# Optimization experiments

Hardware: AMD Instinct MI355X
Metric: run time of the kernel (lower is better)

The kernel has to match this reference:

```python
import jax, jax.numpy as jnp
import numpy as np

# smoothing constants (from init_kwargs)
KERNEL_SIZE = 20
WINDOW = (-10.0, 10.0)
SIGMA = 4.0
AMPLITUDE = 0.5
N_SMOOTH = 331  # 350 - 20 + 1


def setup_inputs() -> dict:
    key = jax.random.key(0)
    ks = jax.random.split(key, 6)
    W, A, M, D = 4000, 64, 6, 500
    wavelengths = jnp.linspace(0.3, 2.5, W, dtype=jnp.float32)  # um
    grid = jnp.linspace(0.25, 2.6, D, dtype=jnp.float32)        # material wavelength tables
    n_tab = 1.3 + 1.5 * jax.random.uniform(ks[0], (M, D), dtype=jnp.float32)
    k_tab = 0.05 * jax.random.uniform(ks[1], (M, D), dtype=jnp.float32)
    fixed_data = jnp.stack([jnp.broadcast_to(grid, (M, D)), n_tab, k_tab], axis=1)  # [M,3,D]
    refractive_index = 1.5 + 1.5 * jax.random.uniform(ks[2], (350,), dtype=jnp.float32)
    compression_ratio = jnp.ones((1,), jnp.float32)
    thickness_above_unk = 0.05 + 0.2 * jax.random.uniform(ks[3], (10,), dtype=jnp.float32)  # um
    thickness_below_unk = 0.05 + 0.2 * jax.random.uniform(ks[4], (9,), dtype=jnp.float32)   # um
    angle_of_incidences = jnp.linspace(0.0, 60.0, A, dtype=jnp.float32)  # degrees
    # stack order: incoming | 10 above | unknown (index M) | 9 below | outgoing
    md = [0] + [1, 2] * 5 + [M] + [3, 4] * 4 + [3] + [5]
    material_distribution = jnp.array(md, dtype=jnp.int32)  # [22]
    unknown_layer_thickness = jnp.array([500.0], jnp.float32)  # nm
    return dict(refractive_index=refractive_index, compression_ratio=compression_ratio,
                fixed_data=fixed_data, thickness_above_unk=thickness_above_unk,
                thickness_below_unk=thickness_below_unk, wavelengths=wavelengths,
                angle_of_incidences=angle_of_incidences,
                material_distribution=material_distribution, polarization=0,
                unknown_layer_thickness=unknown_layer_thickness)


def reference(refractive_index, compression_ratio, fixed_data, thickness_above_unk,
              thickness_below_unk, wavelengths, angle_of_incidences,
              material_distribution, polarization, unknown_layer_thickness):
    D = fixed_data.shape[2]
    n_repeat = D - N_SMOOTH
    # --- gaussian smoothing of the unknown layer's refractive index (valid conv) ---
    x = jnp.linspace(WINDOW[0], WINDOW[1], KERNEL_SIZE)
    g = AMPLITUDE * jnp.exp(-0.5 * (x / SIGMA) ** 2)
    g = (g / jnp.sum(g)).astype(refractive_index.dtype)
    nk_s = jnp.convolve(refractive_index, g, mode='valid')            # [331]
    nk = jnp.concatenate([nk_s, jnp.full((n_repeat,), nk_s[-1], nk_s.dtype)])  # pad to max_data_dim
    dyn_wl = jnp.linspace(jnp.min(wavelengths), jnp.max(wavelengths), N_SMOOTH)
    dyn_wl = jnp.concatenate([dyn_wl, jnp.full((n_repeat,), dyn_wl[-1], dyn_wl.dtype)])
    # --- interpolate all material n,k tables onto the experimental wavelengths ---
    interp = jax.vmap(lambda xp, fp: jnp.interp(wavelengths, xp, fp))
    n_fixc = interp(fixed_data[:, 0], fixed_data[:, 1]) + 1j * interp(fixed_data[:, 0], fixed_data[:, 2])  # [M,W]
    n_unk = jnp.interp(wavelengths, dyn_wl, nk)[None].astype(n_fixc.dtype)  # unknown layer (k=0)
    n_mat = jnp.concatenate([n_fixc, n_unk], axis=0)                  # [M+1, W]
    n_stack = n_mat[material_distribution]                            # [Lyr, W] complex
    # --- thickness list (unknown in nm -> um, scaled by compression ratio) ---
    d_unk = unknown_layer_thickness / 1000.0 * compression_ratio      # [1]
    d = jnp.concatenate([thickness_above_unk, d_unk, thickness_below_unk])  # [L] = [20]
    # --- coherent TMM, vectorized over (angle, wavelength) ---
    th0 = jnp.deg2rad(angle_of_incidences)                            # [A]
    sin0 = (n_stack[0][None, :] * jnp.sin(th0)[:, None])              # [A,W] (Snell invariant)
    sin_th = sin0[None] / n_stack[:, None, :]                         # [Lyr,A,W]
    cos_th = jnp.sqrt(1.0 - sin_th ** 2)
    kz = 2.0 * jnp.pi * n_stack[:, None, :] * cos_th / wavelengths[None, None, :]
    delta = kz[1:-1] * d[:, None, None].astype(kz.dtype)              # [L,A,W]
    nc = n_stack[:, None, :]
    if polarization == 0:  # s-pol
        f = nc * cos_th                                               # [Lyr,A,W]
        r = (f[:-1] - f[1:]) / (f[:-1] + f[1:])                       # [L+1,A,W]
        t = 2.0 * f[:-1] / (f[:-1] + f[1:])
    else:  # p-pol
        num = nc[1:] * cos_th[:-1]
        den = nc[:-1] * cos_th[1:]
        r = (num - den) / (num + den)
        t = 2.0 * nc[:-1, ] * cos_th[:-1] / (num + den)
    # Mtilde = I_0 * prod_j (P_j @ I_j); 2x2 complex recursion via scan
    m00 = 1.0 / t[0]
    m01 = r[0] / t[0]
    m10 = m01
    m11 = m00

    def step(carry, xs):
        c00, c01, c10, c11 = carry
        dl, rj, tj = xs
        em = jnp.exp(-1j * dl) / tj
        ep = jnp.exp(1j * dl) / tj
        a, b, c, dd = em, rj * em, rj * ep, ep
        return (c00 * a + c01 * c, c00 * b + c01 * dd,
                c10 * a + c11 * c, c10 * b + c11 * dd), None

    (m00, m01, m10, m11), _ = jax.lax.scan(step, (m00, m01, m10, m11), (delta, r[1:], t[1:]))
    rr = m10 / m00
    tt = 1.0 / m00
    R = jnp.abs(rr) ** 2                                              # [A,W]
    if polarization == 0:
        f0 = n_stack[0][None] * cos_th[0]
        ff = n_stack[-1][None] * cos_th[-1]
        T = jnp.abs(tt) ** 2 * jnp.real(ff) / jnp.real(f0)
    else:
        T = (jnp.abs(tt) ** 2 * jnp.real(n_stack[-1][None] * jnp.conj(cos_th[-1]))
             / jnp.real(n_stack[0][None] * jnp.conj(cos_th[0])))
    Aabs = 1.0 - R - T
    return jnp.stack([R, T, Aabs])  # [3, A, W]
```

## Files before the change

kernel.cpp:

```cpp
#include <hip/hip_runtime.h>

#define DEV __device__ __forceinline__
#define RCP(x)  __builtin_amdgcn_rcpf(x)
#define SQRT(x) __builtin_amdgcn_sqrtf(x)

constexpr int W_  = 4000;
constexpr int A_  = 64;
constexpr int D_  = 500;
constexpr int NS_ = 331;
constexpr int KS_ = 20;
constexpr int L_  = 22;
constexpr float PIF = 3.14159265358979323846f;

struct cplx { float re, im; };

DEV cplx cmul(cplx a, cplx b) { return { a.re*b.re - a.im*b.im, a.re*b.im + a.im*b.re }; }
DEV cplx cadd(cplx a, cplx b) { return { a.re + b.re, a.im + b.im }; }

DEV cplx cdiv_s(cplx a, cplx b) {
  bool swap = fabsf(b.im) > fabsf(b.re);
  float bl = swap ? b.im : b.re;
  float bs = swap ? b.re : b.im;
  float t   = bs / bl;
  float den = fmaf(bs, t, bl);
  float inv = 1.0f / den;
  float re = swap ? fmaf(a.re, t,  a.im) : fmaf(a.im, t,  a.re);
  float im = swap ? fmaf(a.im, t, -a.re) : fmaf(-a.re, t, a.im);
  return { re * inv, im * inv };
}

DEV cplx csqrtc(cplx z) {
  float x = z.re, y = z.im;
  float mag = SQRT(fmaf(x, x, y * y));
  float t   = SQRT(0.5f * (mag + fabsf(x)));
  float q   = y * 0.5f * RCP(t);
  bool pos  = (x >= 0.0f);
  float re  = pos ? t : fabsf(q);
  float im  = pos ? q : copysignf(t, y);
  return { re, im };
}

__global__ __launch_bounds__(256) void tmm_fused_kernel(
    const float* __restrict__ ri,
    const float* __restrict__ comp,
    const float* __restrict__ fixed,
    const float* __restrict__ tha,
    const float* __restrict__ thb,
    const float* __restrict__ wl,
    const float* __restrict__ ang,
    const int*   __restrict__ md,
    const float* __restrict__ unk,
    float* __restrict__ out)
{
  __shared__ float  s_grid[D_];
  __shared__ float  s_ri[350];
  __shared__ float  s_g[KS_];
  __shared__ int    s_md[L_];
  __shared__ float  s_d[20];
  __shared__ float  s_mn[4], s_mx[4];
  __shared__ float2 s_f[7 * 256];

  const int tid = threadIdx.x;

  for (int i = tid; i < D_;  i += 256) s_grid[i] = fixed[i];
  for (int i = tid; i < 350; i += 256) s_ri[i]   = ri[i];
  if (tid < KS_) {
    float x  = -10.0f + (float)tid * (20.0f / 19.0f);
    float xs = x * 0.25f;
    s_g[tid] = 0.5f * expf(-0.5f * xs * xs);
  }
  if (tid < L_) s_md[tid] = md[tid];
  if (tid < 20)
    s_d[tid] = (tid < 10) ? tha[tid]
             : (tid == 10 ? unk[0] / 1000.0f * comp[0] : thb[tid - 11]);

  float lmin = 3.4e38f, lmax = -3.4e38f;
  for (int i = tid; i < W_; i += 256) {
    float v = wl[i];
    lmin = fminf(lmin, v); lmax = fmaxf(lmax, v);
  }
  #pragma unroll
  for (int o = 32; o; o >>= 1) {
    lmin = fminf(lmin, __shfl_xor(lmin, o, 64));
    lmax = fmaxf(lmax, __shfl_xor(lmax, o, 64));
  }
  if ((tid & 63) == 0) { s_mn[tid >> 6] = lmin; s_mx[tid >> 6] = lmax; }
  __syncthreads();
  const float wmin = fminf(fminf(s_mn[0], s_mn[1]), fminf(s_mn[2], s_mn[3]));
  const float wmax = fmaxf(fmaxf(s_mx[0], s_mx[1]), fmaxf(s_mx[2], s_mx[3]));

  const int a  = blockIdx.y;
  const int w  = blockIdx.x * 256 + tid;
  const int wc = min(w, W_ - 1);
  const float x = wl[wc];

  int lo = 0, hi = D_;
  while (lo < hi) { int mid = (lo + hi) >> 1; if (s_grid[mid] <= x) lo = mid + 1; else hi = mid; }
  const int i = min(max(lo, 1), D_ - 1);
  const float gx0 = s_grid[i - 1];
  const float fr  = (x - gx0) * RCP(s_grid[i] - gx0);
  const bool lowc  = (x < s_grid[0]);
  const bool highc = (x > s_grid[D_ - 1]);

  #pragma unroll
  for (int m = 0; m < 6; ++m) {
    const float* nptr = fixed + (m * 3 + 1) * D_;
    const float* kptr = fixed + (m * 3 + 2) * D_;
    float nv = fmaf(fr, nptr[i] - nptr[i - 1], nptr[i - 1]);
    float kv = fmaf(fr, kptr[i] - kptr[i - 1], kptr[i - 1]);
    if (lowc)  { nv = nptr[0];      kv = kptr[0]; }
    if (highc) { nv = nptr[D_ - 1]; kv = kptr[D_ - 1]; }
    s_f[m * 256 + tid] = make_float2(nv, kv);
  }

  {
    float gsum = 0.0f;
    #pragma unroll
    for (int k = 0; k < KS_; ++k) gsum += s_g[k];
    const float ginv  = 1.0f / gsum;
    const float stepd = (wmax - wmin) / (float)(NS_ - 1);
    const float istep = RCP(stepd);
    int j = (int)floorf((x - wmin) * istep) + 1;
    j = min(max(j, 1), NS_ - 1);
    const int j0 = j - 1;
    float a0 = 0.0f, a1 = 0.0f;
    #pragma unroll
    for (int k = 0; k < KS_; ++k) {
      const float gk = s_g[KS_ - 1 - k];
      a0 = fmaf(s_ri[j0 + k], gk, a0);
      a1 = fmaf(s_ri[j0 + 1 + k], gk, a1);
    }
    a0 *= ginv; a1 *= ginv;
    const float d0 = fmaf((float)j0, stepd, wmin);
    const float d1 = fmaf((float)j,  stepd, wmin);
    const float f  = fmaf((x - d0) * RCP(d1 - d0), a1 - a0, a0);
    s_f[6 * 256 + tid] = make_float2(f, 0.0f);
  }

  const float th0  = ang[a] * (PIF / 180.0f);
  const float s0   = sinf(th0);
  const float klam = 2.0f * PIF * RCP(x);

  const int md0 = s_md[0];
  const float2 nn0 = s_f[md0 * 256 + tid];
  const cplx sin0 = { nn0.x * s0, nn0.y * s0 };

  #pragma unroll
  for (int m = 0; m < 7; ++m) {
    const float2 nn = s_f[m * 256 + tid];
    const float ind = RCP(fmaf(nn.x, nn.x, nn.y * nn.y));
    const cplx invn = { nn.x * ind, -nn.y * ind };
    const cplx st   = cmul(sin0, invn);
    const cplx st2  = cmul(st, st);
    const cplx ct   = csqrtc({ 1.0f - st2.re, -st2.im });
    const cplx f    = cmul({ nn.x, nn.y }, ct);
    s_f[m * 256 + tid] = make_float2(f.re, f.im);
  }

  const float2 f0v = s_f[md0 * 256 + tid];
  const cplx f0 = { f0v.x, f0v.y };

  cplx m00 = {0,0}, m01 = {0,0}, m10 = {0,0}, m11 = {0,0};
  cplx fp = f0;
  {
  }
  float id0 = RCP(fmaf(fp.re, fp.re, fp.im * fp.im));
  cplx ifp = { fp.re * id0, -fp.im * id0 };

  #pragma unroll
  for (int l = 1; l < L_; ++l) {
    const float2 fcv = s_f[s_md[l] * 256 + tid];
    const cplx fc = { fcv.x, fcv.y };
    const cplx q  = cmul(fc, ifp);
    const cplx opq = { 1.0f + q.re,  q.im };
    const cplx tinv = { 0.5f * opq.re, 0.5f * opq.im };
    const float idq = RCP(fmaf(opq.re, opq.re, opq.im * opq.im));
    const cplx omq = { 1.0f - q.re, -q.im };
    const cplx r = { fmaf(omq.re, opq.re,  omq.im * opq.im) * idq,
                     fmaf(omq.im, opq.re, -omq.re * opq.im) * idq };

    if (l == 1) {
      m00 = tinv; m01 = cmul(r, tinv); m10 = m01; m11 = tinv;
    } else {
      const float cst = klam * s_d[l - 2];
      const float dr = fp.re * cst, di = fp.im * cst;
      const float e1 = __expf(di);
      const float e2 = RCP(e1);
      float sn, cs;
      __sincosf(dr, &sn, &cs);
      const cplx em = { e1 * cs, -e1 * sn };
      const cplx ep = { e2 * cs,  e2 * sn };
      const cplx aem = cmul(em, tinv);
      const cplx aep = cmul(ep, tinv);
      const cplx bb  = cmul(r, aem);
      const cplx cc  = cmul(r, aep);
      const cplx t00 = cadd(cmul(m00, aem), cmul(m01, cc));
      const cplx t01 = cadd(cmul(m00, bb),  cmul(m01, aep));
      const cplx t10 = cadd(cmul(m10, aem), cmul(m11, cc));
      const cplx t11 = cadd(cmul(m10, bb),  cmul(m11, aep));
      m00 = t00; m01 = t01; m10 = t10; m11 = t11;
    }
    fp = fc;
    const float idd = RCP(fmaf(fc.re, fc.re, fc.im * fc.im));
    ifp = { fc.re * idd, -fc.im * idd };
  }

  const cplx rr = cdiv_s(m10, m00);
  const cplx tt = cdiv_s({1.0f, 0.0f}, m00);
  const float R = fmaf(rr.re, rr.re, rr.im * rr.im);
  const float T = fmaf(tt.re, tt.re, tt.im * tt.im) * fp.re / f0.re;

  if (w < W_) {
    const int o = a * W_ + w;
    out[o]             = R;
    out[A_ * W_ + o]   = T;
    out[2 * A_ * W_ + o] = 1.0f - R - T;
  }
}

extern "C" void kernel_launch(void* const* d_in, const int* in_sizes, int n_in,
                              void* d_out, int out_size, void* d_ws, size_t ws_size,
                              hipStream_t stream) {
  const float* ri    = (const float*)d_in[0];
  const float* comp  = (const float*)d_in[1];
  const float* fixed = (const float*)d_in[2];
  const float* tha   = (const float*)d_in[3];
  const float* thb   = (const float*)d_in[4];
  const float* wl    = (const float*)d_in[5];
  const float* ang   = (const float*)d_in[6];
  const int*   md    = (const int*)d_in[7];
  const float* unk   = (const float*)d_in[9];
  float* out = (float*)d_out;

  dim3 grid(16, A_);
  tmm_fused_kernel<<<grid, 256, 0, stream>>>(ri, comp, fixed, tha, thb, wl,
                                             ang, md, unk, out);
}
```

Measured before the change: 97.63 us.

## Replace forward transfer-matrix product with backward reflection-coefficient recursion

Drops the 2x2 complex transfer-matrix product in favour of a back-to-front recursion. It carries one effective reflection coefficient and an accumulated transmission factor, so fewer complex multiplies run per layer than for four matrix entries. Inverse admittances are now computed once per material and stored next to each admittance in shared memory, which is widened from float2 to float4. The per-interface factor of 1/2 the old code applied is folded into one constant 2^21 scale on the transmission amplitude. The cost is twice the shared-memory footprint and a complex reciprocal per layer in the recursion.

```diff
diff --git a/kernel.cpp b/kernel.cpp
--- a/kernel.cpp
+++ b/kernel.cpp
@@ -15,18 +15,9 @@
 struct cplx { float re, im; };
 
 DEV cplx cmul(cplx a, cplx b) { return { a.re*b.re - a.im*b.im, a.re*b.im + a.im*b.re }; }
-DEV cplx cadd(cplx a, cplx b) { return { a.re + b.re, a.im + b.im }; }
-
-DEV cplx cdiv_s(cplx a, cplx b) {
-  bool swap = fabsf(b.im) > fabsf(b.re);
-  float bl = swap ? b.im : b.re;
-  float bs = swap ? b.re : b.im;
-  float t   = bs / bl;
-  float den = fmaf(bs, t, bl);
-  float inv = 1.0f / den;
-  float re = swap ? fmaf(a.re, t,  a.im) : fmaf(a.im, t,  a.re);
-  float im = swap ? fmaf(a.im, t, -a.re) : fmaf(-a.re, t, a.im);
-  return { re * inv, im * inv };
+DEV cplx cinv(cplx z) {
+  float d = RCP(fmaf(z.re, z.re, z.im * z.im));
+  return { z.re * d, -z.im * d };
 }
 
 DEV cplx csqrtc(cplx z) {
@@ -58,7 +49,7 @@
   __shared__ int    s_md[L_];
   __shared__ float  s_d[20];
   __shared__ float  s_mn[4], s_mx[4];
-  __shared__ float2 s_f[7 * 256];
+  __shared__ float4 s_f[7 * 256];
 
   const int tid = threadIdx.x;
 
@@ -110,7 +101,7 @@
     float kv = fmaf(fr, kptr[i] - kptr[i - 1], kptr[i - 1]);
     if (lowc)  { nv = nptr[0];      kv = kptr[0]; }
     if (highc) { nv = nptr[D_ - 1]; kv = kptr[D_ - 1]; }
-    s_f[m * 256 + tid] = make_float2(nv, kv);
+    s_f[m * 256 + tid] = make_float4(nv, kv, 0.0f, 0.0f);
   }
 
   {
@@ -134,7 +125,7 @@
     const float d0 = fmaf((float)j0, stepd, wmin);
     const float d1 = fmaf((float)j,  stepd, wmin);
     const float f  = fmaf((x - d0) * RCP(d1 - d0), a1 - a0, a0);
-    s_f[6 * 256 + tid] = make_float2(f, 0.0f);
+    s_f[6 * 256 + tid] = make_float4(f, 0.0f, 0.0f, 0.0f);
   }
 
   const float th0  = ang[a] * (PIF / 180.0f);
@@ -142,78 +133,68 @@
   const float klam = 2.0f * PIF * RCP(x);
 
   const int md0 = s_md[0];
-  const float2 nn0 = s_f[md0 * 256 + tid];
+  const float4 nn0 = s_f[md0 * 256 + tid];
   const cplx sin0 = { nn0.x * s0, nn0.y * s0 };
 
   #pragma unroll
   for (int m = 0; m < 7; ++m) {
-    const float2 nn = s_f[m * 256 + tid];
-    const float ind = RCP(fmaf(nn.x, nn.x, nn.y * nn.y));
-    const cplx invn = { nn.x * ind, -nn.y * ind };
+    const float4 nn = s_f[m * 256 + tid];
+    const cplx invn = cinv({ nn.x, nn.y });
     const cplx st   = cmul(sin0, invn);
     const cplx st2  = cmul(st, st);
     const cplx ct   = csqrtc({ 1.0f - st2.re, -st2.im });
     const cplx f    = cmul({ nn.x, nn.y }, ct);
-    s_f[m * 256 + tid] = make_float2(f.re, f.im);
-  }
-
-  const float2 f0v = s_f[md0 * 256 + tid];
-  const cplx f0 = { f0v.x, f0v.y };
-
-  cplx m00 = {0,0}, m01 = {0,0}, m10 = {0,0}, m11 = {0,0};
-  cplx fp = f0;
-  {
-  }
-  float id0 = RCP(fmaf(fp.re, fp.re, fp.im * fp.im));
-  cplx ifp = { fp.re * id0, -fp.im * id0 };
-
-  #pragma unroll
-  for (int l = 1; l < L_; ++l) {
-    const float2 fcv = s_f[s_md[l] * 256 + tid];
-    const cplx fc = { fcv.x, fcv.y };
-    const cplx q  = cmul(fc, ifp);
-    const cplx opq = { 1.0f + q.re,  q.im };
-    const cplx tinv = { 0.5f * opq.re, 0.5f * opq.im };
-    const float idq = RCP(fmaf(opq.re, opq.re, opq.im * opq.im));
-    const cplx omq = { 1.0f - q.re, -q.im };
-    const cplx r = { fmaf(omq.re, opq.re,  omq.im * opq.im) * idq,
-                     fmaf(omq.im, opq.re, -omq.re * opq.im) * idq };
-
-    if (l == 1) {
-      m00 = tinv; m01 = cmul(r, tinv); m10 = m01; m11 = tinv;
-    } else {
-      const float cst = klam * s_d[l - 2];
-      const float dr = fp.re * cst, di = fp.im * cst;
-      const float e1 = __expf(di);
-      const float e2 = RCP(e1);
-      float sn, cs;
-      __sincosf(dr, &sn, &cs);
-      const cplx em = { e1 * cs, -e1 * sn };
-      const cplx ep = { e2 * cs,  e2 * sn };
-      const cplx aem = cmul(em, tinv);
-      const cplx aep = cmul(ep, tinv);
-      const cplx bb  = cmul(r, aem);
-      const cplx cc  = cmul(r, aep);
-      const cplx t00 = cadd(cmul(m00, aem), cmul(m01, cc));
-      const cplx t01 = cadd(cmul(m00, bb),  cmul(m01, aep));
-      const cplx t10 = cadd(cmul(m10, aem), cmul(m11, cc));
-      const cplx t11 = cadd(cmul(m10, bb),  cmul(m11, aep));
-      m00 = t00; m01 = t01; m10 = t10; m11 = t11;
-    }
-    fp = fc;
-    const float idd = RCP(fmaf(fc.re, fc.re, fc.im * fc.im));
-    ifp = { fc.re * idd, -fc.im * idd };
-  }
-
-  const cplx rr = cdiv_s(m10, m00);
-  const cplx tt = cdiv_s({1.0f, 0.0f}, m00);
+    const cplx fi   = cinv(f);
+    s_f[m * 256 + tid] = make_float4(f.re, f.im, fi.re, fi.im);
+  }
+
+  cplx u   = { 0.0f, 0.0f };
+  cplx tac = { 1.0f, 0.0f };
+  float4 fdn = s_f[s_md[L_ - 1] * 256 + tid];
+  const float fL_re = fdn.x;
+
+  #pragma unroll
+  for (int j = L_ - 2; j >= 1; --j) {
+    const float4 fj = s_f[s_md[j] * 256 + tid];
+    const cplx q   = cmul({ fdn.x, fdn.y }, { fj.z, fj.w });
+    const cplx iop = cinv({ 1.0f + q.re, q.im });
+    const cplx r   = cmul({ 1.0f - q.re, -q.im }, iop);
+
+    const float cst = klam * s_d[j - 1];
+    const float dr = fj.x * cst, di = fj.y * cst;
+    const float e2 = __expf(-di);
+    float sn, cs;
+    __sincosf(dr, &sn, &cs);
+    const cplx ph   = { e2 * cs, e2 * sn };
+    const cplx beta = cmul(ph, ph);
+
+    const cplx ru  = cmul(r, u);
+    const cplx idn = cinv({ 1.0f + ru.re, ru.im });
+    tac = cmul(tac, cmul(cmul(iop, ph), idn));
+    u = cmul(beta, cmul({ r.re + u.re, r.im + u.im }, idn));
+
+    fdn = fj;
+  }
+
+  const float4 f0v = s_f[md0 * 256 + tid];
+  const cplx q0   = cmul({ fdn.x, fdn.y }, { f0v.z, f0v.w });
+  const cplx iop0 = cinv({ 1.0f + q0.re, q0.im });
+  const cplx r0   = cmul({ 1.0f - q0.re, -q0.im }, iop0);
+  const cplx ru0  = cmul(r0, u);
+  const cplx idn0 = cinv({ 1.0f + ru0.re, ru0.im });
+  const cplx rr   = cmul({ r0.re + u.re, r0.im + u.im }, idn0);
+  cplx tt = cmul(cmul(iop0, idn0), tac);
+
+  const float SC = 2097152.0f;
+  tt.re *= SC; tt.im *= SC;
+
   const float R = fmaf(rr.re, rr.re, rr.im * rr.im);
-  const float T = fmaf(tt.re, tt.re, tt.im * tt.im) * fp.re / f0.re;
+  const float T = fmaf(tt.re, tt.re, tt.im * tt.im) * fL_re * RCP(f0v.x);
 
   if (w < W_) {
     const int o = a * W_ + w;
-    out[o]             = R;
-    out[A_ * W_ + o]   = T;
+    out[o]               = R;
+    out[A_ * W_ + o]     = T;
     out[2 * A_ * W_ + o] = 1.0f - R - T;
   }
 }
```

Measured after the change: 97.37 us. About the same (-0.3%).
